# Optimization experiments

Measured on AMD Instinct MI355X. Metric: run time of the kernel, lower is better.

The kernel has to match this reference:

```python
import jax, jax.numpy as jnp
import numpy as np

IMG_W, IMG_H = 960.0, 512.0          # NETWORK.IMAGE_SIZE
HM_W, HM_H = 240.0, 128.0            # NETWORK.HEATMAP_SIZE (w, h)
GRID_SIZE = (8000.0, 8000.0, 2000.0)
CUBE = (80, 80, 20)
SPACE_CENTER = (0.0, -500.0, 800.0)


def _make_grid():
    # compute_grid: meshgrid(indexing='ij'), flattened to [nbins, 3]
    gx = np.linspace(-GRID_SIZE[0] / 2, GRID_SIZE[0] / 2, CUBE[0]) + SPACE_CENTER[0]
    gy = np.linspace(-GRID_SIZE[1] / 2, GRID_SIZE[1] / 2, CUBE[1]) + SPACE_CENTER[1]
    gz = np.linspace(-GRID_SIZE[2] / 2, GRID_SIZE[2] / 2, CUBE[2]) + SPACE_CENTER[2]
    X, Y, Z = np.meshgrid(gx, gy, gz, indexing='ij')
    return jnp.asarray(np.stack([X.ravel(), Y.ravel(), Z.ravel()], 1), jnp.float32)


def setup_inputs() -> dict:
    key = jax.random.key(0)
    ks = jax.random.split(key, 8)
    n, B, J, H, W = 5, 4, 15, 128, 240
    heatmaps = jax.random.uniform(ks[0], (n, B, J, H, W), jnp.float32)
    # cameras: rotate about z per view, positioned so all grid points have depth > 0
    thetas = np.linspace(0.0, 2 * np.pi, n, endpoint=False)
    Rs = np.zeros((n, B, 3, 3), np.float32)
    for v, th in enumerate(thetas):
        c, s = np.cos(th), np.sin(th)
        Rs[v, :] = np.array([[c, -s, 0.0], [s, c, 0.0], [0.0, 0.0, 1.0]], np.float32)
    cam_R = jnp.asarray(Rs)
    cam_T = jnp.asarray(np.tile(np.array([0.0, 0.0, -5000.0], np.float32), (n, B, 1))) \
        + 50.0 * jax.random.normal(ks[1], (n, B, 3), jnp.float32)
    cam_f = 1500.0 + 20.0 * jax.random.normal(ks[2], (n, B, 2), jnp.float32)
    cam_c = jnp.asarray([IMG_W / 2, IMG_H / 2], jnp.float32) \
        + 5.0 * jax.random.normal(ks[3], (n, B, 2), jnp.float32)
    cam_k = jnp.asarray(np.tile(np.array([-0.01, 0.001, 0.0], np.float32), (n, B, 1))) \
        + 1e-4 * jax.random.normal(ks[4], (n, B, 3), jnp.float32)
    cam_p = 1e-3 * jax.random.normal(ks[5], (n, B, 2), jnp.float32)
    center = jnp.asarray([IMG_W / 2, IMG_H / 2], jnp.float32) \
        + 10.0 * jax.random.normal(ks[6], (n, B, 2), jnp.float32)
    scale = jnp.asarray([IMG_W / 200.0, IMG_H / 200.0], jnp.float32) \
        * (1.0 + 0.05 * jax.random.uniform(ks[7], (n, B, 2), jnp.float32))
    return {"heatmaps": heatmaps, "cam_R": cam_R, "cam_T": cam_T, "cam_f": cam_f,
            "cam_c": cam_c, "cam_k": cam_k, "cam_p": cam_p, "center": center,
            "scale": scale}


def _forward(heatmaps, cam_R, cam_T, cam_f, cam_c, cam_k, cam_p, center, scale):
    n, B, J, Hd, Wd = heatmaps.shape
    grid = _make_grid()                                   # [N, 3]
    N = grid.shape[0]
    # --- project_pose (pinhole + radial/tangential distortion) ---
    diff = grid[None, None] - cam_T[:, :, None, :]        # [v,b,N,3]
    xcam = jnp.einsum('vbij,vbnj->vbni', cam_R, diff)     # [v,b,N,3]
    y = xcam[..., :2] / (xcam[..., 2:3] + 1e-5)
    r2 = jnp.sum(y * y, -1)                               # [v,b,N]
    radial = 1.0 + cam_k[..., 0:1] * r2 + cam_k[..., 1:2] * r2 ** 2 + cam_k[..., 2:3] * r2 ** 3
    tan = cam_p[..., 0:1] * y[..., 1] + cam_p[..., 1:2] * y[..., 0]
    y = y * (radial + 2.0 * tan)[..., None] \
        + jnp.stack([cam_p[..., 1], cam_p[..., 0]], -1)[:, :, None, :] * r2[..., None]
    pix = cam_f[:, :, None, :] * y + cam_c[:, :, None, :]  # [v,b,N,2]
    # --- bounding: inside image of size (width, height) = 2*center ---
    wh = 2.0 * center                                      # [v,b,2]
    bounding = ((pix[..., 0] >= 0) & (pix[..., 1] >= 0)
                & (pix[..., 0] < wh[..., 0:1]) & (pix[..., 1] < wh[..., 1:2])
                ).astype(heatmaps.dtype)                   # [v,b,N]
    maxwh = jnp.maximum(wh[..., 0], wh[..., 1])[..., None, None]
    pix = jnp.clip(pix, -1.0, maxwh)
    # --- get_transform(center, scale, 0, img_size) + do_transform ---
    hs = 200.0 * scale                                     # [v,b,2]
    img = jnp.asarray([IMG_W, IMG_H], heatmaps.dtype)
    t_scale = img / hs                                     # diag of affine
    t_off = img * (-center / hs + 0.5)
    xy = pix * t_scale[:, :, None, :] + t_off[:, :, None, :]
    # scale to heatmap resolution, then to normalized [-1,1] (align_corners=True)
    xy = xy * (jnp.asarray([HM_W, HM_H], heatmaps.dtype) / img)
    sg = xy / jnp.asarray([HM_W - 1, HM_H - 1], heatmaps.dtype) * 2.0 - 1.0
    sg = jnp.clip(sg, -1.1, 1.1)
    # --- bilinear grid_sample, align_corners=True, zeros padding ---
    px = (sg[..., 0] + 1.0) * 0.5 * (Wd - 1)
    py = (sg[..., 1] + 1.0) * 0.5 * (Hd - 1)
    x0 = jnp.floor(px)
    y0 = jnp.floor(py)
    wx = px - x0
    wy = py - y0
    x0i = x0.astype(jnp.int32)
    y0i = y0.astype(jnp.int32)
    flat = heatmaps.reshape(n, B, J, Hd * Wd)

    def corner(xi, yi):
        valid = ((xi >= 0) & (xi < Wd) & (yi >= 0) & (yi < Hd)).astype(heatmaps.dtype)
        idx = jnp.clip(yi, 0, Hd - 1) * Wd + jnp.clip(xi, 0, Wd - 1)   # [v,b,N]
        g = jnp.take_along_axis(flat, idx[:, :, None, :], axis=3)       # [v,b,J,N]
        return g * valid[:, :, None, :]

    val = (corner(x0i, y0i) * ((1 - wx) * (1 - wy))[:, :, None, :]
           + corner(x0i + 1, y0i) * (wx * (1 - wy))[:, :, None, :]
           + corner(x0i, y0i + 1) * ((1 - wx) * wy)[:, :, None, :]
           + corner(x0i + 1, y0i + 1) * (wx * wy)[:, :, None, :])       # [v,b,J,N]
    # --- per-view cube = bounding * sampled; combine over views ---
    cubes_v = bounding[:, :, None, :] * val
    num = jnp.sum(cubes_v * bounding[:, :, None, :], axis=0)            # [b,J,N]
    den = jnp.sum(bounding, axis=0)[:, None, :] + 1e-6
    cubes = jnp.clip(num / den, 0.0, 1.0).reshape(B, J, CUBE[0], CUBE[1], CUBE[2])
    grids = jnp.broadcast_to(grid, (B, N, 3))
    return cubes, grids


def reference(heatmaps, cam_R, cam_T, cam_f, cam_c, cam_k, cam_p, center, scale):
    return _forward(heatmaps, cam_R, cam_T, cam_f, cam_c, cam_k, cam_p, center, scale)
```

## Files before the change

kernel.cpp:

```cpp
#include <hip/hip_runtime.h>
#include <hip/hip_fp16.h>

#define NV 5
#define NB 4
#define NJ 15
#define HD 128
#define WD 240
#define CX 80
#define CY 80
#define CZ 20
#define NPTS (CX*CY*CZ)
#define JP16 16
#define BLOCKS_PER_B (NPTS/256)
#define NWG (NB*BLOCKS_PER_B)

struct ViewSample {
    float w[4];
    int   cx0, cx1, cy0, cy1;
    float bnd;
};

__device__ __forceinline__ ViewSample project_one_view(
    float gx, float gy, float gz,
    const float* __restrict__ cam_R, const float* __restrict__ cam_T,
    const float* __restrict__ cam_f, const float* __restrict__ cam_c,
    const float* __restrict__ cam_k, const float* __restrict__ cam_p,
    const float* __restrict__ center, const float* __restrict__ scale,
    int cb)
{
    const float* R = cam_R + cb*9;
    const float* T = cam_T + cb*3;
    float fx = cam_f[cb*2+0], fy = cam_f[cb*2+1];
    float ccx = cam_c[cb*2+0], ccy = cam_c[cb*2+1];
    float k0 = cam_k[cb*3+0], k1 = cam_k[cb*3+1], k2 = cam_k[cb*3+2];
    float p0 = cam_p[cb*2+0], p1 = cam_p[cb*2+1];
    float cenx = center[cb*2+0], ceny = center[cb*2+1];
    float scx = scale[cb*2+0],  scy = scale[cb*2+1];

    float dx = gx - T[0], dy = gy - T[1], dz = gz - T[2];
    float xc = R[0]*dx + R[1]*dy + R[2]*dz;
    float yc = R[3]*dx + R[4]*dy + R[5]*dz;
    float zc = R[6]*dx + R[7]*dy + R[8]*dz;
    float invz = 1.0f / (zc + 1e-5f);
    float ux = xc * invz, uy = yc * invz;
    float r2 = ux*ux + uy*uy;
    float radial = 1.0f + k0*r2 + k1*(r2*r2) + k2*(r2*r2*r2);
    float tn = p0*uy + p1*ux;
    float m  = radial + 2.0f*tn;
    float xd = ux*m + p1*r2;
    float yd = uy*m + p0*r2;
    float pixx = fx*xd + ccx;
    float pixy = fy*yd + ccy;

    float whx = 2.0f*cenx, why = 2.0f*ceny;
    float bnd = (pixx >= 0.0f && pixy >= 0.0f && pixx < whx && pixy < why) ? 1.0f : 0.0f;
    float mwh = fmaxf(whx, why);
    pixx = fminf(fmaxf(pixx, -1.0f), mwh);
    pixy = fminf(fmaxf(pixy, -1.0f), mwh);

    float hsx = 200.0f*scx, hsy = 200.0f*scy;
    float xyx = (pixx * (960.0f/hsx) + 960.0f*(-cenx/hsx + 0.5f)) * 0.25f;
    float xyy = (pixy * (512.0f/hsy) + 512.0f*(-ceny/hsy + 0.5f)) * 0.25f;
    float sgx = (xyx / 239.0f) * 2.0f - 1.0f;
    float sgy = (xyy / 127.0f) * 2.0f - 1.0f;
    sgx = fminf(fmaxf(sgx, -1.1f), 1.1f);
    sgy = fminf(fmaxf(sgy, -1.1f), 1.1f);

    float pxf = (sgx + 1.0f) * 0.5f * 239.0f;
    float pyf = (sgy + 1.0f) * 0.5f * 127.0f;
    float x0f = floorf(pxf), y0f = floorf(pyf);
    float wx = pxf - x0f, wy = pyf - y0f;
    int x0 = (int)x0f, y0 = (int)y0f;
    int x1 = x0 + 1,   y1 = y0 + 1;
    float vx0 = (x0 >= 0 && x0 < WD) ? 1.0f : 0.0f;
    float vx1 = (x1 >= 0 && x1 < WD) ? 1.0f : 0.0f;
    float vy0 = (y0 >= 0 && y0 < HD) ? 1.0f : 0.0f;
    float vy1 = (y1 >= 0 && y1 < HD) ? 1.0f : 0.0f;

    ViewSample s;
    s.cx0 = min(max(x0, 0), WD-1);
    s.cx1 = min(max(x1, 0), WD-1);
    s.cy0 = min(max(y0, 0), HD-1);
    s.cy1 = min(max(y1, 0), HD-1);
    s.w[0] = (1.0f-wx)*(1.0f-wy) * vx0*vy0 * bnd;
    s.w[1] = wx*(1.0f-wy)        * vx1*vy0 * bnd;
    s.w[2] = (1.0f-wx)*wy        * vx0*vy1 * bnd;
    s.w[3] = wx*wy               * vx1*vy1 * bnd;
    s.bnd = bnd;
    return s;
}

__device__ __forceinline__ void grid_coords(int nn, float& gx, float& gy, float& gz) {
    int iz = nn % CZ;
    int iy = (nn / CZ) % CY;
    int ix = nn / (CZ*CY);
    gx = (float)(((double)ix * (8000.0/79.0) - 4000.0) + 0.0);
    gy = (float)(((double)iy * (8000.0/79.0) - 4000.0) - 500.0);
    gz = (float)(((double)iz * (2000.0/19.0) - 1000.0) + 800.0);
}

__global__ __launch_bounds__(256) void hm_transpose_f16(
    const float* __restrict__ hm, __half* __restrict__ out)
{
    int idx = blockIdx.x * 256 + threadIdx.x;
    if (idx >= NV*NB*HD*WD) return;
    int x  = idx % WD;
    int y  = (idx / WD) % HD;
    int vb = idx / (WD*HD);
    const float* src = hm + ((size_t)vb*NJ*HD + (size_t)y)*WD + x;
    union { float4 f4[2]; __half h[16]; } u;
    #pragma unroll
    for (int j = 0; j < NJ; ++j) u.h[j] = __float2half(src[(size_t)j*HD*WD]);
    u.h[15] = __float2half(0.0f);
    float4* dst = reinterpret_cast<float4*>(out + (size_t)idx * JP16);
    dst[0] = u.f4[0];
    dst[1] = u.f4[1];
}

__global__ __launch_bounds__(256) void project_kernel_f16(
    const __half* __restrict__ hmT,
    const float* __restrict__ cam_R, const float* __restrict__ cam_T,
    const float* __restrict__ cam_f, const float* __restrict__ cam_c,
    const float* __restrict__ cam_k, const float* __restrict__ cam_p,
    const float* __restrict__ center, const float* __restrict__ scale,
    float* __restrict__ out_cubes, float* __restrict__ out_grids)
{
    int wg   = (int)blockIdx.x;
    int swz  = (wg % 8) * (NWG/8) + wg / 8;
    const int b  = swz / BLOCKS_PER_B;
    const int nn = (swz % BLOCKS_PER_B)*256 + threadIdx.x;

    float gx, gy, gz;
    grid_coords(nn, gx, gy, gz);

    float wts[NV][4];
    int   offs[NV][4];
    float den = 0.0f;

    #pragma unroll
    for (int v = 0; v < NV; ++v) {
        int cb = v*NB + b;
        ViewSample s = project_one_view(gx, gy, gz, cam_R, cam_T, cam_f, cam_c,
                                        cam_k, cam_p, center, scale, cb);
        wts[v][0] = s.w[0]; wts[v][1] = s.w[1];
        wts[v][2] = s.w[2]; wts[v][3] = s.w[3];
        int base = cb * (HD*WD*JP16);
        offs[v][0] = base + (s.cy0*WD + s.cx0)*JP16;
        offs[v][1] = base + (s.cy0*WD + s.cx1)*JP16;
        offs[v][2] = base + (s.cy1*WD + s.cx0)*JP16;
        offs[v][3] = base + (s.cy1*WD + s.cx1)*JP16;
        den += s.bnd;
    }

    float acc[NJ];
    #pragma unroll
    for (int j = 0; j < NJ; ++j) acc[j] = 0.0f;

    #pragma unroll
    for (int v = 0; v < NV; ++v) {
        float wsum = wts[v][0] + wts[v][1] + wts[v][2] + wts[v][3];
        if (__any(wsum > 0.0f)) {
            #pragma unroll
            for (int c = 0; c < 4; ++c) {
                float w = wts[v][c];
                if (w != 0.0f) {
                    union { float4 f4[2]; __half2 h2[8]; } u;
                    const float4* p = reinterpret_cast<const float4*>(hmT + offs[v][c]);
                    u.f4[0] = p[0];
                    u.f4[1] = p[1];
                    #pragma unroll
                    for (int k = 0; k < 7; ++k) {
                        float2 f = __half22float2(u.h2[k]);
                        acc[2*k]   += w * f.x;
                        acc[2*k+1] += w * f.y;
                    }
                    float2 f7 = __half22float2(u.h2[7]);
                    acc[14] += w * f7.x;
                }
            }
        }
    }

    float inv_den = 1.0f / (den + 1e-6f);
    #pragma unroll
    for (int j = 0; j < NJ; ++j) {
        float val = fminf(fmaxf(acc[j]*inv_den, 0.0f), 1.0f);
        out_cubes[((size_t)b*NJ + j)*NPTS + nn] = val;
    }
    float* g = out_grids + ((size_t)b*NPTS + nn)*3;
    g[0] = gx; g[1] = gy; g[2] = gz;
}

__global__ __launch_bounds__(256) void project_kernel_direct(
    const float* __restrict__ hm,
    const float* __restrict__ cam_R, const float* __restrict__ cam_T,
    const float* __restrict__ cam_f, const float* __restrict__ cam_c,
    const float* __restrict__ cam_k, const float* __restrict__ cam_p,
    const float* __restrict__ center, const float* __restrict__ scale,
    float* __restrict__ out_cubes, float* __restrict__ out_grids)
{
    const int b  = blockIdx.x / BLOCKS_PER_B;
    const int nn = (blockIdx.x % BLOCKS_PER_B)*256 + threadIdx.x;

    float gx, gy, gz;
    grid_coords(nn, gx, gy, gz);

    float wts[NV][4];
    int   offs[NV][4];
    float den = 0.0f;

    #pragma unroll
    for (int v = 0; v < NV; ++v) {
        int cb = v*NB + b;
        ViewSample s = project_one_view(gx, gy, gz, cam_R, cam_T, cam_f, cam_c,
                                        cam_k, cam_p, center, scale, cb);
        wts[v][0] = s.w[0]; wts[v][1] = s.w[1];
        wts[v][2] = s.w[2]; wts[v][3] = s.w[3];
        offs[v][0] = s.cy0*WD + s.cx0;
        offs[v][1] = s.cy0*WD + s.cx1;
        offs[v][2] = s.cy1*WD + s.cx0;
        offs[v][3] = s.cy1*WD + s.cx1;
        den += s.bnd;
    }

    float acc[NJ];
    #pragma unroll
    for (int j = 0; j < NJ; ++j) acc[j] = 0.0f;

    #pragma unroll
    for (int v = 0; v < NV; ++v) {
        float wsum = wts[v][0] + wts[v][1] + wts[v][2] + wts[v][3];
        if (__any(wsum > 0.0f)) {
            int cb = v*NB + b;
            #pragma unroll
            for (int j = 0; j < NJ; ++j) {
                const float* base = hm + ((size_t)cb*NJ + j)*(HD*WD);
                acc[j] += wts[v][0]*base[offs[v][0]] + wts[v][1]*base[offs[v][1]]
                        + wts[v][2]*base[offs[v][2]] + wts[v][3]*base[offs[v][3]];
            }
        }
    }

    float inv_den = 1.0f / (den + 1e-6f);
    #pragma unroll
    for (int j = 0; j < NJ; ++j) {
        float val = fminf(fmaxf(acc[j]*inv_den, 0.0f), 1.0f);
        out_cubes[((size_t)b*NJ + j)*NPTS + nn] = val;
    }
    float* g = out_grids + ((size_t)b*NPTS + nn)*3;
    g[0] = gx; g[1] = gy; g[2] = gz;
}

extern "C" void kernel_launch(void* const* d_in, const int* in_sizes, int n_in,
                              void* d_out, int out_size, void* d_ws, size_t ws_size,
                              hipStream_t stream) {
    const float* hm     = (const float*)d_in[0];
    const float* cam_R  = (const float*)d_in[1];
    const float* cam_T  = (const float*)d_in[2];
    const float* cam_f  = (const float*)d_in[3];
    const float* cam_c  = (const float*)d_in[4];
    const float* cam_k  = (const float*)d_in[5];
    const float* cam_p  = (const float*)d_in[6];
    const float* center = (const float*)d_in[7];
    const float* scale  = (const float*)d_in[8];

    float* out_cubes = (float*)d_out;
    float* out_grids = out_cubes + (size_t)NB*NJ*NPTS;

    size_t need = (size_t)NV*NB*HD*WD*JP16*sizeof(__half);
    if (ws_size >= need) {
        __half* hmT = (__half*)d_ws;
        hipLaunchKernelGGL(hm_transpose_f16,
                           dim3((NV*NB*HD*WD)/256), dim3(256), 0, stream, hm, hmT);
        hipLaunchKernelGGL(project_kernel_f16,
                           dim3(NWG), dim3(256), 0, stream,
                           hmT, cam_R, cam_T, cam_f, cam_c, cam_k, cam_p,
                           center, scale, out_cubes, out_grids);
    } else {
        hipLaunchKernelGGL(project_kernel_direct,
                           dim3(NWG), dim3(256), 0, stream,
                           hm, cam_R, cam_T, cam_f, cam_c, cam_k, cam_p,
                           center, scale, out_cubes, out_grids);
    }
}
```

Before: 125.8 us.

## Vectorize heatmap transpose to four pixels per thread and fuse per-view projection-gather loop

The transpose kernel now has each thread read float4 vectors across four adjacent pixels for all joints and write 64 halves, replacing scalar loads. This widens memory transactions and cuts the thread count by four. The projection kernels merge the projection and gather phases into one non-unrolled per-view loop, which lowers register pressure from the per-view weight and offset arrays. The risk is less instruction-level parallelism across views.

```diff
diff --git a/kernel.cpp b/kernel.cpp
--- a/kernel.cpp
+++ b/kernel.cpp
@@ -99,22 +99,37 @@
     gz = (float)(((double)iz * (2000.0/19.0) - 1000.0) + 800.0);
 }
 
-__global__ __launch_bounds__(256) void hm_transpose_f16(
+__global__ __launch_bounds__(256) void hm_transpose_f16x4(
     const float* __restrict__ hm, __half* __restrict__ out)
 {
     int idx = blockIdx.x * 256 + threadIdx.x;
-    if (idx >= NV*NB*HD*WD) return;
-    int x  = idx % WD;
-    int y  = (idx / WD) % HD;
-    int vb = idx / (WD*HD);
-    const float* src = hm + ((size_t)vb*NJ*HD + (size_t)y)*WD + x;
-    union { float4 f4[2]; __half h[16]; } u;
-    #pragma unroll
-    for (int j = 0; j < NJ; ++j) u.h[j] = __float2half(src[(size_t)j*HD*WD]);
-    u.h[15] = __float2half(0.0f);
-    float4* dst = reinterpret_cast<float4*>(out + (size_t)idx * JP16);
-    dst[0] = u.f4[0];
-    dst[1] = u.f4[1];
+    if (idx >= NV*NB*HD*(WD/4)) return;
+    int xq = idx % (WD/4);
+    int y  = (idx / (WD/4)) % HD;
+    int vb = idx / ((WD/4)*HD);
+    const float* src = hm + ((size_t)vb*NJ*HD + (size_t)y)*WD + xq*4;
+
+    float4 ld[NJ];
+    #pragma unroll
+    for (int j = 0; j < NJ; ++j)
+        ld[j] = *reinterpret_cast<const float4*>(src + (size_t)j*HD*WD);
+
+    union { float4 f4[8]; __half h[64]; } u;
+    #pragma unroll
+    for (int j = 0; j < NJ; ++j) {
+        u.h[0*JP16 + j] = __float2half(ld[j].x);
+        u.h[1*JP16 + j] = __float2half(ld[j].y);
+        u.h[2*JP16 + j] = __float2half(ld[j].z);
+        u.h[3*JP16 + j] = __float2half(ld[j].w);
+    }
+    u.h[0*JP16 + 15] = __float2half(0.0f);
+    u.h[1*JP16 + 15] = __float2half(0.0f);
+    u.h[2*JP16 + 15] = __float2half(0.0f);
+    u.h[3*JP16 + 15] = __float2half(0.0f);
+
+    float4* dst = reinterpret_cast<float4*>(out + (size_t)idx * 64);
+    #pragma unroll
+    for (int q = 0; q < 8; ++q) dst[q] = u.f4[q];
 }
 
 __global__ __launch_bounds__(256) void project_kernel_f16(
@@ -133,39 +148,31 @@
     float gx, gy, gz;
     grid_coords(nn, gx, gy, gz);
 
-    float wts[NV][4];
-    int   offs[NV][4];
+    float acc[NJ];
+    #pragma unroll
+    for (int j = 0; j < NJ; ++j) acc[j] = 0.0f;
     float den = 0.0f;
 
-    #pragma unroll
+    #pragma unroll 1
     for (int v = 0; v < NV; ++v) {
         int cb = v*NB + b;
         ViewSample s = project_one_view(gx, gy, gz, cam_R, cam_T, cam_f, cam_c,
                                         cam_k, cam_p, center, scale, cb);
-        wts[v][0] = s.w[0]; wts[v][1] = s.w[1];
-        wts[v][2] = s.w[2]; wts[v][3] = s.w[3];
-        int base = cb * (HD*WD*JP16);
-        offs[v][0] = base + (s.cy0*WD + s.cx0)*JP16;
-        offs[v][1] = base + (s.cy0*WD + s.cx1)*JP16;
-        offs[v][2] = base + (s.cy1*WD + s.cx0)*JP16;
-        offs[v][3] = base + (s.cy1*WD + s.cx1)*JP16;
         den += s.bnd;
-    }
-
-    float acc[NJ];
-    #pragma unroll
-    for (int j = 0; j < NJ; ++j) acc[j] = 0.0f;
-
-    #pragma unroll
-    for (int v = 0; v < NV; ++v) {
-        float wsum = wts[v][0] + wts[v][1] + wts[v][2] + wts[v][3];
+        float wsum = s.w[0] + s.w[1] + s.w[2] + s.w[3];
         if (__any(wsum > 0.0f)) {
+            int base = cb * (HD*WD*JP16);
+            int off[4];
+            off[0] = base + (s.cy0*WD + s.cx0)*JP16;
+            off[1] = base + (s.cy0*WD + s.cx1)*JP16;
+            off[2] = base + (s.cy1*WD + s.cx0)*JP16;
+            off[3] = base + (s.cy1*WD + s.cx1)*JP16;
             #pragma unroll
             for (int c = 0; c < 4; ++c) {
-                float w = wts[v][c];
+                float w = s.w[c];
                 if (w != 0.0f) {
                     union { float4 f4[2]; __half2 h2[8]; } u;
-                    const float4* p = reinterpret_cast<const float4*>(hmT + offs[v][c]);
+                    const float4* p = reinterpret_cast<const float4*>(hmT + off[c]);
                     u.f4[0] = p[0];
                     u.f4[1] = p[1];
                     #pragma unroll
@@ -205,38 +212,29 @@
     float gx, gy, gz;
     grid_coords(nn, gx, gy, gz);
 
-    float wts[NV][4];
-    int   offs[NV][4];
+    float acc[NJ];
+    #pragma unroll
+    for (int j = 0; j < NJ; ++j) acc[j] = 0.0f;
     float den = 0.0f;
 
-    #pragma unroll
+    #pragma unroll 1
     for (int v = 0; v < NV; ++v) {
         int cb = v*NB + b;
         ViewSample s = project_one_view(gx, gy, gz, cam_R, cam_T, cam_f, cam_c,
                                         cam_k, cam_p, center, scale, cb);
-        wts[v][0] = s.w[0]; wts[v][1] = s.w[1];
-        wts[v][2] = s.w[2]; wts[v][3] = s.w[3];
-        offs[v][0] = s.cy0*WD + s.cx0;
-        offs[v][1] = s.cy0*WD + s.cx1;
-        offs[v][2] = s.cy1*WD + s.cx0;
-        offs[v][3] = s.cy1*WD + s.cx1;
         den += s.bnd;
-    }
-
-    float acc[NJ];
-    #pragma unroll
-    for (int j = 0; j < NJ; ++j) acc[j] = 0.0f;
-
-    #pragma unroll
-    for (int v = 0; v < NV; ++v) {
-        float wsum = wts[v][0] + wts[v][1] + wts[v][2] + wts[v][3];
+        float wsum = s.w[0] + s.w[1] + s.w[2] + s.w[3];
         if (__any(wsum > 0.0f)) {
-            int cb = v*NB + b;
+            int off[4];
+            off[0] = s.cy0*WD + s.cx0;
+            off[1] = s.cy0*WD + s.cx1;
+            off[2] = s.cy1*WD + s.cx0;
+            off[3] = s.cy1*WD + s.cx1;
             #pragma unroll
             for (int j = 0; j < NJ; ++j) {
                 const float* base = hm + ((size_t)cb*NJ + j)*(HD*WD);
-                acc[j] += wts[v][0]*base[offs[v][0]] + wts[v][1]*base[offs[v][1]]
-                        + wts[v][2]*base[offs[v][2]] + wts[v][3]*base[offs[v][3]];
+                acc[j] += s.w[0]*base[off[0]] + s.w[1]*base[off[1]]
+                        + s.w[2]*base[off[2]] + s.w[3]*base[off[3]];
             }
         }
     }
@@ -270,8 +268,8 @@
     size_t need = (size_t)NV*NB*HD*WD*JP16*sizeof(__half);
     if (ws_size >= need) {
         __half* hmT = (__half*)d_ws;
-        hipLaunchKernelGGL(hm_transpose_f16,
-                           dim3((NV*NB*HD*WD)/256), dim3(256), 0, stream, hm, hmT);
+        hipLaunchKernelGGL(hm_transpose_f16x4,
+                           dim3((NV*NB*HD*(WD/4))/256), dim3(256), 0, stream, hm, hmT);
         hipLaunchKernelGGL(project_kernel_f16,
                            dim3(NWG), dim3(256), 0, stream,
                            hmT, cam_R, cam_T, cam_f, cam_c, cam_k, cam_p,
```

After: 129.6 us. 3.1% more time.
